# Kernel tuning notes

Hardware: AMD Instinct MI355X
Metric: run time of the kernel (lower is better)

## Reference

```python
import jax, jax.numpy as jnp
import numpy as np

N, E, IN_DIM, H, D = 50000, 1600000, 128, 4, 32
LEAKY_ALPHA = 0.2

def _glorot(key, shape):
    r = np.sqrt(6.0 / (shape[0] + shape[1]))
    return jax.random.uniform(key, shape, jnp.float32, -r, r)

def setup_inputs() -> dict:
    key = jax.random.key(0)
    ks = jax.random.split(key, 6)
    x = jax.random.normal(ks[0], (N, IN_DIM), jnp.float32)
    edge_index = jax.random.randint(ks[1], (2, E), 0, N, jnp.int64 if jax.config.jax_enable_x64 else jnp.int32)
    W_src = _glorot(ks[2], (IN_DIM, H * D))
    W_dst = _glorot(ks[3], (IN_DIM, H * D))
    W_val = _glorot(ks[4], (IN_DIM, H * D))
    attn_vec = _glorot(ks[5], (1, H)).reshape(1, H, 1) * jnp.ones((1, H, D), jnp.float32)
    # faithful glorot for (1,H,D): fan based on shape[0]+shape[1]=1+H as in source
    r = np.sqrt(6.0 / (1 + H))
    attn_vec = jax.random.uniform(jax.random.fold_in(key, 7), (1, H, D), jnp.float32, -r, r)
    return {"x": x, "edge_index": edge_index, "W_src": W_src, "W_dst": W_dst, "W_val": W_val, "attn_vec": attn_vec}

def reference(x, edge_index, W_src, W_dst, W_val, attn_vec):
    n = x.shape[0]
    h = attn_vec.shape[1]
    d = attn_vec.shape[2]
    h_s = (x @ W_src).reshape(n, h, d)
    h_d = (x @ W_dst).reshape(n, h, d)
    h_v = (x @ W_val).reshape(n, h, d)
    src, dst = edge_index[0], edge_index[1]
    # GATv2 edge scores: a^T LeakyReLU(W_src h_i + W_dst h_j)  -> [E, H]
    middle = jax.nn.leaky_relu(h_s[src] + h_d[dst], negative_slope=LEAKY_ALPHA)
    scores = jnp.sum(middle * attn_vec, axis=-1)  # [E, H]
    # segment softmax over incoming edges of each dst node (all heads at once)
    seg_max = jax.ops.segment_max(scores, dst, num_segments=n)  # [N, H]
    exp_scores = jnp.exp(scores - seg_max[dst])
    seg_sum = jax.ops.segment_sum(exp_scores, dst, num_segments=n)
    attn = exp_scores / (seg_sum[dst] + 1e-9)  # [E, H]
    # weighted message aggregation
    messages = (attn[..., None] * h_v[src]).reshape(-1, h * d)  # [E, H*D]
    out_sum = jax.ops.segment_sum(messages, dst, num_segments=n)  # [N, H*D]
    return out_sum, attn
```

## Files before the change

### kernel.cpp

```cpp
#include <hip/hip_runtime.h>

#define LEAKY 0.2f
#define BCAP 512

typedef __attribute__((ext_vector_type(8))) short short8v;
typedef __attribute__((ext_vector_type(4))) float f32x4;
typedef _Float16 half2v __attribute__((ext_vector_type(2)));

__device__ __forceinline__ float h2f(unsigned short b) {
    union { unsigned short u; _Float16 h; } c; c.u = b; return (float)c.h;
}
__device__ __forceinline__ unsigned short f2h(float f) {
    union { unsigned short u; _Float16 h; } c; c.h = (_Float16)f; return c.u;
}
__device__ __forceinline__ half2v u2h2(unsigned u) {
    union { unsigned u; half2v h; } c; c.u = u; return c.h;
}
__device__ __forceinline__ void h4w(unsigned wx, unsigned wy, float& a, float& b, float& c, float& d) {
    a = h2f((unsigned short)(wx & 0xFFFF)); b = h2f((unsigned short)(wx >> 16));
    c = h2f((unsigned short)(wy & 0xFFFF)); d = h2f((unsigned short)(wy >> 16));
}
__device__ __forceinline__ unsigned short f2bf(float f) {
    unsigned u = __float_as_uint(f);
    return (unsigned short)((u + 0x7FFFu + ((u >> 16) & 1u)) >> 16);
}
__device__ __forceinline__ float bf2f(unsigned short b) {
    return __uint_as_float((unsigned)b << 16);
}
__device__ __forceinline__ int clampi(int v, int hi) { return v < 0 ? 0 : (v > hi ? hi : v); }
__device__ __forceinline__ int ld_idx(const int* __restrict__ ei, int is64, size_t pos) {
    return is64 ? ei[pos * 2] : ei[pos];
}
__device__ __forceinline__ half2v h2max(half2v a, half2v b) {
#if __has_builtin(__builtin_elementwise_max)
    return __builtin_elementwise_max(a, b);
#else
    half2v r; r.x = a.x > b.x ? a.x : b.x; r.y = a.y > b.y ? a.y : b.y; return r;
#endif
}
__device__ __forceinline__ half2v h2min(half2v a, half2v b) {
#if __has_builtin(__builtin_elementwise_min)
    return __builtin_elementwise_min(a, b);
#else
    half2v r; r.x = a.x < b.x ? a.x : b.x; r.y = a.y < b.y ? a.y : b.y; return r;
#endif
}
__device__ __forceinline__ float fdot2f(half2v a, half2v b, float c) {
#if __has_builtin(__builtin_amdgcn_fdot2)
    return __builtin_amdgcn_fdot2(a, b, c, false);
#else
    return (float)a.x * (float)b.x + (float)a.y * (float)b.y + c;
#endif
}

__global__ __launch_bounds__(256) void prep_kernel(
    const int* __restrict__ ei, int* __restrict__ iflag,
    int* __restrict__ bcnt, int NB8,
    const float* __restrict__ W0, const float* __restrict__ W1, const float* __restrict__ W2,
    uint4* __restrict__ wfrag)
{
    const int b = blockIdx.x;
    if (b == 0) {
        __shared__ int nz;
        if (threadIdx.x == 0) nz = 0;
        __syncthreads();
        if (ei[2 * threadIdx.x + 1] != 0) atomicOr(&nz, 1);
        __syncthreads();
        if (threadIdx.x == 0) *iflag = (nz == 0) ? 1 : 0;
    } else if (b <= 24) {
        int t = (b - 1) * 256 + threadIdx.x;
        int lane = t & 63, ks = (t >> 6) & 3, nt = (t >> 8) & 7, w = t >> 11;
        const float* W = (w == 0) ? W0 : ((w == 1) ? W1 : W2);
        int col = nt * 16 + (lane & 15);
        int k0 = ks * 32 + ((lane >> 4) & 3) * 8;
        short8v h, l;
        #pragma unroll
        for (int j = 0; j < 8; ++j) {
            float v = W[(size_t)(k0 + j) * 128 + col];
            unsigned short hb = f2bf(v);
            h[j] = (short)hb;
            l[j] = (short)f2bf(v - bf2f(hb));
        }
        size_t slot = ((size_t)nt * 4 + ks) * 64 + lane;
        *(short8v*)&wfrag[(size_t)w * 4096 + 0 * 2048 + slot] = h;
        *(short8v*)&wfrag[(size_t)w * 4096 + 1 * 2048 + slot] = l;
    } else {
        int t = (b - 25) * 256 + threadIdx.x;
        if (t < NB8) bcnt[t] = 0;
    }
}

__global__ __launch_bounds__(256) void bucket_scatter_kernel(
    const int* __restrict__ ei, const int* __restrict__ iflag,
    int* __restrict__ bcnt, uint2* __restrict__ bucket_data, int N, int E)
{
    int t = blockIdx.x * 256 + threadIdx.x;
    if (t >= E) return;
    int is64 = *iflag;
    int src = clampi(ld_idx(ei, is64, (size_t)t), N - 1);
    int dst = clampi(ld_idx(ei, is64, (size_t)E + t), N - 1);
    int slot = (dst >> 6) * 8 + (blockIdx.x & 7);
    int k = atomicAdd(&bcnt[slot], 1);
    if (k < BCAP)
        bucket_data[(size_t)slot * BCAP + k] =
            make_uint2((unsigned)src | ((unsigned)(dst & 63) << 16), (unsigned)t);
}

__global__ __launch_bounds__(256) void bscan_kernel(
    const int* __restrict__ bcnt, int* __restrict__ bbase,
    int* __restrict__ offs, int NB, int N, int E)
{
    __shared__ int buf[256];
    __shared__ int base;
    const int t = threadIdx.x;
    if (t == 0) { base = 0; bbase[0] = 0; offs[N] = E; }
    __syncthreads();
    for (int start = 0; start < NB; start += 256) {
        int i = start + t;
        int v = 0;
        if (i < NB) {
            #pragma unroll
            for (int s = 0; s < 8; ++s) {
                int c = bcnt[i * 8 + s];
                v += (c < BCAP ? c : BCAP);
            }
        }
        buf[t] = v;
        __syncthreads();
        #pragma unroll
        for (int off = 1; off < 256; off <<= 1) {
            int xv = (t >= off) ? buf[t - off] : 0;
            __syncthreads();
            buf[t] += xv;
            __syncthreads();
        }
        if (i < NB) bbase[i + 1] = base + buf[t];
        __syncthreads();
        if (t == 0) base += buf[255];
        __syncthreads();
    }
}

__global__ __launch_bounds__(256) void csr_build_kernel(
    const uint2* __restrict__ bucket_data, const int* __restrict__ bcnt,
    const int* __restrict__ bbase, int* __restrict__ offs,
    int2* __restrict__ sorted2, int N)
{
    __shared__ uint2 ebuf[8 * BCAP];
    __shared__ int cnt[64];
    __shared__ int pre[64];
    __shared__ int soff[9];
    const int b = blockIdx.x;
    const int t = threadIdx.x;
    if (t == 0) {
        int acc = 0;
        #pragma unroll
        for (int s = 0; s < 8; ++s) {
            soff[s] = acc;
            int c = bcnt[b * 8 + s];
            acc += (c < BCAP ? c : BCAP);
        }
        soff[8] = acc;
    }
    if (t < 64) cnt[t] = 0;
    __syncthreads();
    const int tcnt = soff[8];
    #pragma unroll
    for (int s = 0; s < 8; ++s) {
        int o = soff[s], c = soff[s + 1] - o;
        const uint2* p = &bucket_data[((size_t)b * 8 + s) * BCAP];
        for (int k = t; k < c; k += 256) ebuf[o + k] = p[k];
    }
    __syncthreads();
    for (int k = t; k < tcnt; k += 256)
        atomicAdd(&cnt[(ebuf[k].x >> 16) & 63], 1);
    __syncthreads();
    const int gbase = bbase[b];
    if (t < 64) {
        int v = cnt[t], o = v;
        #pragma unroll
        for (int off = 1; off < 64; off <<= 1) {
            int xv = __shfl_up(v, off);
            if (t >= off) v += xv;
        }
        pre[t] = v - o;
        int node = b * 64 + t;
        if (node < N) offs[node] = gbase + pre[t];
    }
    __syncthreads();
    if (t < 64) cnt[t] = pre[t];
    __syncthreads();
    for (int k = t; k < tcnt; k += 256) {
        uint2 d = ebuf[k];
        int dl = (d.x >> 16) & 63;
        int pos = gbase + atomicAdd(&cnt[dl], 1);
        sorted2[pos] = make_int2((int)(d.x & 0xFFFF), (int)d.y);
    }
}

__global__ __launch_bounds__(256) void gemm3_mfma_kernel(
    const float* __restrict__ x, const uint4* __restrict__ wfrag,
    unsigned short* __restrict__ comb_us, float* __restrict__ hd, int N)
{
    __shared__ uint4 wsb4[4096];
    unsigned short* wsb = (unsigned short*)wsb4;
    const int tid = threadIdx.x;
    const int wave = tid >> 6;
    const int lane = tid & 63;
    const int lhi = lane >> 4;
    const int llo = lane & 15;
    const int base_row = blockIdx.x * 128 + wave * 32;

    short8v Ahi[2][4], Alo[2][4];
    #pragma unroll
    for (int rt = 0; rt < 2; ++rt) {
        #pragma unroll
        for (int ks = 0; ks < 4; ++ks) {
            int row = base_row + rt * 16 + llo;
            int rowc = row < N ? row : N - 1;
            const float* p = &x[(size_t)rowc * 128 + ks * 32 + lhi * 8];
            float4 v0 = *(const float4*)p;
            float4 v1 = *(const float4*)(p + 4);
            float vv[8] = {v0.x, v0.y, v0.z, v0.w, v1.x, v1.y, v1.z, v1.w};
            short8v h, l;
            #pragma unroll
            for (int j = 0; j < 8; ++j) {
                unsigned short hb = f2bf(vv[j]);
                h[j] = (short)hb;
                l[j] = (short)f2bf(vv[j] - bf2f(hb));
            }
            Ahi[rt][ks] = h; Alo[rt][ks] = l;
        }
    }

    for (int w = 0; w < 3; ++w) {
        __syncthreads();
        #pragma unroll
        for (int it = 0; it < 16; ++it) {
            int slot = it * 256 + tid;
            wsb4[slot] = wfrag[(size_t)w * 4096 + slot];
        }
        __syncthreads();

        f32x4 acc[2][8];
        #pragma unroll
        for (int rt = 0; rt < 2; ++rt)
            #pragma unroll
            for (int nt = 0; nt < 8; ++nt)
                acc[rt][nt] = (f32x4){0.f, 0.f, 0.f, 0.f};

        #pragma unroll
        for (int ks = 0; ks < 4; ++ks) {
            #pragma unroll
            for (int nt = 0; nt < 8; ++nt) {
                short8v Bh = *(short8v*)&wsb[((((size_t)0 * 8 + nt) * 4 + ks) * 64 + lane) * 8];
                short8v Bl = *(short8v*)&wsb[((((size_t)1 * 8 + nt) * 4 + ks) * 64 + lane) * 8];
                acc[0][nt] = __builtin_amdgcn_mfma_f32_16x16x32_bf16(Ahi[0][ks], Bh, acc[0][nt], 0, 0, 0);
                acc[1][nt] = __builtin_amdgcn_mfma_f32_16x16x32_bf16(Ahi[1][ks], Bh, acc[1][nt], 0, 0, 0);
                acc[0][nt] = __builtin_amdgcn_mfma_f32_16x16x32_bf16(Alo[0][ks], Bh, acc[0][nt], 0, 0, 0);
                acc[1][nt] = __builtin_amdgcn_mfma_f32_16x16x32_bf16(Alo[1][ks], Bh, acc[1][nt], 0, 0, 0);
                acc[0][nt] = __builtin_amdgcn_mfma_f32_16x16x32_bf16(Ahi[0][ks], Bl, acc[0][nt], 0, 0, 0);
                acc[1][nt] = __builtin_amdgcn_mfma_f32_16x16x32_bf16(Ahi[1][ks], Bl, acc[1][nt], 0, 0, 0);
            }
        }

        #pragma unroll
        for (int rt = 0; rt < 2; ++rt) {
            #pragma unroll
            for (int nt = 0; nt < 8; ++nt) {
                #pragma unroll
                for (int reg = 0; reg < 4; ++reg) {
                    int node = base_row + rt * 16 + lhi * 4 + reg;
                    int col = nt * 16 + llo;
                    if (node < N) {
                        float v = acc[rt][nt][reg];
                        if (w == 1) {
                            hd[(size_t)node * 128 + col] = v;
                        } else {
                            int slot = (w == 2) ? 1 : 0;
                            comb_us[(size_t)node * 256 + (col >> 2) * 8 + slot * 4 + (col & 3)] = f2h(v);
                        }
                    }
                }
            }
        }
    }
}

__global__ __launch_bounds__(256) void gather_fused_kernel(
    const int* __restrict__ offs, const int2* __restrict__ sorted2,
    const uint4* __restrict__ comb, const float* __restrict__ hd,
    const float* __restrict__ av,
    float* __restrict__ scores, float* __restrict__ out,
    float* __restrict__ segsum, int N)
{
    int wid = (int)(((size_t)blockIdx.x * 256 + threadIdx.x) >> 6);
    if (wid >= N) return;
    int lane = threadIdx.x & 63;
    int sub = lane >> 5;
    int le = lane & 31;
    int h = le >> 3;
    int beg = offs[wid], end = offs[wid + 1];

    float4 d4 = *(const float4*)&hd[(size_t)wid * 128 + le * 4];
    float4 a4 = *(const float4*)&av[le * 4];
    const half2v d2_0 = {(_Float16)d4.x, (_Float16)d4.y};
    const half2v d2_1 = {(_Float16)d4.z, (_Float16)d4.w};
    const half2v av2_0 = {(_Float16)a4.x, (_Float16)a4.y};
    const half2v av2_1 = {(_Float16)a4.z, (_Float16)a4.w};
    const half2v hz = {(_Float16)0.f, (_Float16)0.f};

    float sum = 0.f;
    float a0 = 0.f, a1 = 0.f, a2 = 0.f, a3 = 0.f;

    int j = beg + sub;
    int2 se0 = make_int2(0, 0), se1 = make_int2(0, 0);
    uint4 c0 = make_uint4(0, 0, 0, 0);
    if (j < end)     se0 = sorted2[j];
    if (j + 2 < end) se1 = sorted2[j + 2];
    if (j < end)     c0 = comb[(size_t)se0.x * 32 + le];

    while (j < end) {
        int jn = j + 2;
        int2 se2 = make_int2(0, 0);
        uint4 c1 = make_uint4(0, 0, 0, 0);
        if (jn + 2 < end) se2 = sorted2[jn + 2];
        if (jn < end)     c1 = comb[(size_t)se1.x * 32 + le];

        half2v m0 = u2h2(c0.x) + d2_0;
        half2v m1 = u2h2(c0.y) + d2_1;
        half2v p0 = h2max(m0, hz), q0 = h2min(m0, hz);
        half2v p1 = h2max(m1, hz), q1 = h2min(m1, hz);
        float sp = fdot2f(p1, av2_1, fdot2f(p0, av2_0, 0.f));
        float sq = fdot2f(q1, av2_1, fdot2f(q0, av2_0, 0.f));
        float s = fmaf(LEAKY, sq, sp);
        s += __shfl_xor(s, 1);
        s += __shfl_xor(s, 2);
        s += __shfl_xor(s, 4);
        float w = __expf(s);
        if ((le & 7) == 0) scores[(size_t)se0.y * 4 + h] = w;
        sum += w;
        float v0, v1, v2, v3;
        h4w(c0.z, c0.w, v0, v1, v2, v3);
        a0 += w * v0; a1 += w * v1; a2 += w * v2; a3 += w * v3;

        j = jn; se0 = se1; se1 = se2; c0 = c1;
    }
    sum += __shfl_xor(sum, 32);
    a0 += __shfl_xor(a0, 32); a1 += __shfl_xor(a1, 32);
    a2 += __shfl_xor(a2, 32); a3 += __shfl_xor(a3, 32);
    float inv = 1.f / (sum + 1e-9f);
    if (sub == 0) {
        *(float4*)&out[(size_t)wid * 128 + le * 4] =
            make_float4(a0 * inv, a1 * inv, a2 * inv, a3 * inv);
        if ((le & 7) == 0) segsum[(size_t)wid * 4 + h] = inv;
    }
}

__global__ __launch_bounds__(256) void attn_write_kernel(
    const int* __restrict__ ei, const int* __restrict__ iflag,
    float* sc, const float* __restrict__ segsum, int N, int E)
{
    int t = blockIdx.x * 256 + threadIdx.x;
    if (t >= E * 4) return;
    int e = t >> 2, h = t & 3;
    int dst = clampi(ld_idx(ei, *iflag, (size_t)E + e), N - 1);
    sc[t] = sc[t] * segsum[(size_t)dst * 4 + h];
}

extern "C" void kernel_launch(void* const* d_in, const int* in_sizes, int n_in,
                              void* d_out, int out_size, void* d_ws, size_t ws_size,
                              hipStream_t stream)
{
    const float* x  = (const float*)d_in[0];
    const int* ei   = (const int*)d_in[1];
    const float* W0 = (const float*)d_in[2];
    const float* W1 = (const float*)d_in[3];
    const float* W2 = (const float*)d_in[4];
    const float* av = (const float*)d_in[5];
    const int N = in_sizes[0] / 128;
    const int E = in_sizes[1] / 2;
    const int NB = (N + 63) >> 6;

    float* out_f = (float*)d_out;
    float* hd = out_f;
    float* out_sum = out_f;
    float* scores = out_f + (size_t)N * 128;

    uint2* bucket_data = (uint2*)d_ws;
    uint4* comb = (uint4*)d_ws;
    size_t ubytes = ((size_t)NB * 8 * BCAP * 8 + 255) & ~(size_t)255;
    int2* sorted2 = (int2*)((char*)d_ws + ubytes);
    float* segsum = (float*)(sorted2 + (size_t)E);
    int* bcnt = (int*)(segsum + (size_t)N * 4);
    int* bbase = bcnt + NB * 8;
    int* offs = bbase + (NB + 1);
    int* iflag = offs + (N + 1);
    uint4* wfrag = (uint4*)(((uintptr_t)(iflag + 1) + 255) & ~(uintptr_t)255);

    const int zblocks = (NB * 8 + 255) / 256;
    prep_kernel<<<25 + zblocks, 256, 0, stream>>>(ei, iflag, bcnt, NB * 8, W0, W1, W2, wfrag);
    bucket_scatter_kernel<<<(E + 255) / 256, 256, 0, stream>>>(
        ei, iflag, bcnt, bucket_data, N, E);
    bscan_kernel<<<1, 256, 0, stream>>>(bcnt, bbase, offs, NB, N, E);
    csr_build_kernel<<<NB, 256, 0, stream>>>(bucket_data, bcnt, bbase, offs, sorted2, N);
    gemm3_mfma_kernel<<<(N + 127) / 128, 256, 0, stream>>>(
        x, wfrag, (unsigned short*)comb, hd, N);
    gather_fused_kernel<<<(N + 3) / 4, 256, 0, stream>>>(
        offs, sorted2, comb, hd, av, scores, out_sum, segsum, N);
    attn_write_kernel<<<(E * 4 + 255) / 256, 256, 0, stream>>>(
        ei, iflag, scores, segsum, N, E);
}
```

Before: 379.5 us.

## Fuse attention normalization into gather kernel and alias bucket buffer into output

Removes the separate attn_write kernel: each node's wave now rescales its own edges' scores by the inverse segment sum right after aggregation, using the CSR edge ids instead of rereading edge_index and a segsum array. The GEMM is moved before bucketing, and the bucket staging buffer now lives in the scores region of the output, which shrinks workspace use and avoids a separate allocation. The bscan kernel uses 1024 threads and BCAP drops to 511. This relies on the waitcnt and intra-wave ordering so that each score is written before it is rescaled, and the rescale does scattered read-modify-writes on scores.

```diff
diff --git a/kernel.cpp b/kernel.cpp
--- a/kernel.cpp
+++ b/kernel.cpp
@@ -1,7 +1,7 @@
 #include <hip/hip_runtime.h>
 
 #define LEAKY 0.2f
-#define BCAP 512
+#define BCAP 511
 
 typedef __attribute__((ext_vector_type(8))) short short8v;
 typedef __attribute__((ext_vector_type(4))) float f32x4;
@@ -87,114 +87,6 @@
     } else {
         int t = (b - 25) * 256 + threadIdx.x;
         if (t < NB8) bcnt[t] = 0;
-    }
-}
-
-__global__ __launch_bounds__(256) void bucket_scatter_kernel(
-    const int* __restrict__ ei, const int* __restrict__ iflag,
-    int* __restrict__ bcnt, uint2* __restrict__ bucket_data, int N, int E)
-{
-    int t = blockIdx.x * 256 + threadIdx.x;
-    if (t >= E) return;
-    int is64 = *iflag;
-    int src = clampi(ld_idx(ei, is64, (size_t)t), N - 1);
-    int dst = clampi(ld_idx(ei, is64, (size_t)E + t), N - 1);
-    int slot = (dst >> 6) * 8 + (blockIdx.x & 7);
-    int k = atomicAdd(&bcnt[slot], 1);
-    if (k < BCAP)
-        bucket_data[(size_t)slot * BCAP + k] =
-            make_uint2((unsigned)src | ((unsigned)(dst & 63) << 16), (unsigned)t);
-}
-
-__global__ __launch_bounds__(256) void bscan_kernel(
-    const int* __restrict__ bcnt, int* __restrict__ bbase,
-    int* __restrict__ offs, int NB, int N, int E)
-{
-    __shared__ int buf[256];
-    __shared__ int base;
-    const int t = threadIdx.x;
-    if (t == 0) { base = 0; bbase[0] = 0; offs[N] = E; }
-    __syncthreads();
-    for (int start = 0; start < NB; start += 256) {
-        int i = start + t;
-        int v = 0;
-        if (i < NB) {
-            #pragma unroll
-            for (int s = 0; s < 8; ++s) {
-                int c = bcnt[i * 8 + s];
-                v += (c < BCAP ? c : BCAP);
-            }
-        }
-        buf[t] = v;
-        __syncthreads();
-        #pragma unroll
-        for (int off = 1; off < 256; off <<= 1) {
-            int xv = (t >= off) ? buf[t - off] : 0;
-            __syncthreads();
-            buf[t] += xv;
-            __syncthreads();
-        }
-        if (i < NB) bbase[i + 1] = base + buf[t];
-        __syncthreads();
-        if (t == 0) base += buf[255];
-        __syncthreads();
-    }
-}
-
-__global__ __launch_bounds__(256) void csr_build_kernel(
-    const uint2* __restrict__ bucket_data, const int* __restrict__ bcnt,
-    const int* __restrict__ bbase, int* __restrict__ offs,
-    int2* __restrict__ sorted2, int N)
-{
-    __shared__ uint2 ebuf[8 * BCAP];
-    __shared__ int cnt[64];
-    __shared__ int pre[64];
-    __shared__ int soff[9];
-    const int b = blockIdx.x;
-    const int t = threadIdx.x;
-    if (t == 0) {
-        int acc = 0;
-        #pragma unroll
-        for (int s = 0; s < 8; ++s) {
-            soff[s] = acc;
-            int c = bcnt[b * 8 + s];
-            acc += (c < BCAP ? c : BCAP);
-        }
-        soff[8] = acc;
-    }
-    if (t < 64) cnt[t] = 0;
-    __syncthreads();
-    const int tcnt = soff[8];
-    #pragma unroll
-    for (int s = 0; s < 8; ++s) {
-        int o = soff[s], c = soff[s + 1] - o;
-        const uint2* p = &bucket_data[((size_t)b * 8 + s) * BCAP];
-        for (int k = t; k < c; k += 256) ebuf[o + k] = p[k];
-    }
-    __syncthreads();
-    for (int k = t; k < tcnt; k += 256)
-        atomicAdd(&cnt[(ebuf[k].x >> 16) & 63], 1);
-    __syncthreads();
-    const int gbase = bbase[b];
-    if (t < 64) {
-        int v = cnt[t], o = v;
-        #pragma unroll
-        for (int off = 1; off < 64; off <<= 1) {
-            int xv = __shfl_up(v, off);
-            if (t >= off) v += xv;
-        }
-        pre[t] = v - o;
-        int node = b * 64 + t;
-        if (node < N) offs[node] = gbase + pre[t];
-    }
-    __syncthreads();
-    if (t < 64) cnt[t] = pre[t];
-    __syncthreads();
-    for (int k = t; k < tcnt; k += 256) {
-        uint2 d = ebuf[k];
-        int dl = (d.x >> 16) & 63;
-        int pos = gbase + atomicAdd(&cnt[dl], 1);
-        sorted2[pos] = make_int2((int)(d.x & 0xFFFF), (int)d.y);
     }
 }
 
@@ -287,12 +179,119 @@
     }
 }
 
+__global__ __launch_bounds__(256) void bucket_scatter_kernel(
+    const int* __restrict__ ei, const int* __restrict__ iflag,
+    int* __restrict__ bcnt, uint2* __restrict__ bucket_data, int N, int E)
+{
+    int t = blockIdx.x * 256 + threadIdx.x;
+    if (t >= E) return;
+    int is64 = *iflag;
+    int src = clampi(ld_idx(ei, is64, (size_t)t), N - 1);
+    int dst = clampi(ld_idx(ei, is64, (size_t)E + t), N - 1);
+    int slot = (dst >> 6) * 8 + (blockIdx.x & 7);
+    int k = atomicAdd(&bcnt[slot], 1);
+    if (k < BCAP)
+        bucket_data[(size_t)slot * BCAP + k] =
+            make_uint2((unsigned)src | ((unsigned)(dst & 63) << 16), (unsigned)t);
+}
+
+__global__ __launch_bounds__(1024) void bscan_kernel(
+    const int* __restrict__ bcnt, int* __restrict__ bbase,
+    int* __restrict__ offs, int NB, int N, int E)
+{
+    __shared__ int buf[1024];
+    __shared__ int base;
+    const int t = threadIdx.x;
+    if (t == 0) { base = 0; bbase[0] = 0; offs[N] = E; }
+    __syncthreads();
+    for (int start = 0; start < NB; start += 1024) {
+        int i = start + t;
+        int v = 0;
+        if (i < NB) {
+            #pragma unroll
+            for (int s = 0; s < 8; ++s) {
+                int c = bcnt[i * 8 + s];
+                v += (c < BCAP ? c : BCAP);
+            }
+        }
+        buf[t] = v;
+        __syncthreads();
+        #pragma unroll
+        for (int off = 1; off < 1024; off <<= 1) {
+            int xv = (t >= off) ? buf[t - off] : 0;
+            __syncthreads();
+            buf[t] += xv;
+            __syncthreads();
+        }
+        if (i < NB) bbase[i + 1] = base + buf[t];
+        __syncthreads();
+        if (t == 0) base += buf[1023];
+        __syncthreads();
+    }
+}
+
+__global__ __launch_bounds__(256) void csr_build_kernel(
+    const uint2* __restrict__ bucket_data, const int* __restrict__ bcnt,
+    const int* __restrict__ bbase, int* __restrict__ offs,
+    int2* __restrict__ sorted2, int N)
+{
+    __shared__ uint2 ebuf[8 * BCAP];
+    __shared__ int cnt[64];
+    __shared__ int pre[64];
+    __shared__ int soff[9];
+    const int b = blockIdx.x;
+    const int t = threadIdx.x;
+    if (t == 0) {
+        int acc = 0;
+        #pragma unroll
+        for (int s = 0; s < 8; ++s) {
+            soff[s] = acc;
+            int c = bcnt[b * 8 + s];
+            acc += (c < BCAP ? c : BCAP);
+        }
+        soff[8] = acc;
+    }
+    if (t < 64) cnt[t] = 0;
+    __syncthreads();
+    const int tcnt = soff[8];
+    #pragma unroll
+    for (int s = 0; s < 8; ++s) {
+        int o = soff[s], c = soff[s + 1] - o;
+        const uint2* p = &bucket_data[((size_t)b * 8 + s) * BCAP];
+        for (int k = t; k < c; k += 256) ebuf[o + k] = p[k];
+    }
+    __syncthreads();
+    for (int k = t; k < tcnt; k += 256)
+        atomicAdd(&cnt[(ebuf[k].x >> 16) & 63], 1);
+    __syncthreads();
+    const int gbase = bbase[b];
+    if (t < 64) {
+        int v = cnt[t], o = v;
+        #pragma unroll
+        for (int off = 1; off < 64; off <<= 1) {
+            int xv = __shfl_up(v, off);
+            if (t >= off) v += xv;
+        }
+        pre[t] = v - o;
+        int node = b * 64 + t;
+        if (node < N) offs[node] = gbase + pre[t];
+    }
+    __syncthreads();
+    if (t < 64) cnt[t] = pre[t];
+    __syncthreads();
+    for (int k = t; k < tcnt; k += 256) {
+        uint2 d = ebuf[k];
+        int dl = (d.x >> 16) & 63;
+        int pos = gbase + atomicAdd(&cnt[dl], 1);
+        sorted2[pos] = make_int2((int)(d.x & 0xFFFF), (int)d.y);
+    }
+}
+
 __global__ __launch_bounds__(256) void gather_fused_kernel(
     const int* __restrict__ offs, const int2* __restrict__ sorted2,
     const uint4* __restrict__ comb, const float* __restrict__ hd,
     const float* __restrict__ av,
-    float* __restrict__ scores, float* __restrict__ out,
-    float* __restrict__ segsum, int N)
+    float* __restrict__ scores, float* __restrict__ out, int N)
 {
     int wid = (int)(((size_t)blockIdx.x * 256 + threadIdx.x) >> 6);
     if (wid >= N) return;
@@ -353,19 +352,15 @@
     if (sub == 0) {
         *(float4*)&out[(size_t)wid * 128 + le * 4] =
             make_float4(a0 * inv, a1 * inv, a2 * inv, a3 * inv);
-        if ((le & 7) == 0) segsum[(size_t)wid * 4 + h] = inv;
-    }
-}
-
-__global__ __launch_bounds__(256) void attn_write_kernel(
-    const int* __restrict__ ei, const int* __restrict__ iflag,
-    float* sc, const float* __restrict__ segsum, int N, int E)
-{
-    int t = blockIdx.x * 256 + threadIdx.x;
-    if (t >= E * 4) return;
-    int e = t >> 2, h = t & 3;
-    int dst = clampi(ld_idx(ei, *iflag, (size_t)E + e), N - 1);
-    sc[t] = sc[t] * segsum[(size_t)dst * 4 + h];
+    }
+
+    asm volatile("s_waitcnt vmcnt(0)" ::: "memory");
+    float invh = __shfl(inv, (lane & 3) * 8);
+    for (int j2 = beg + (lane >> 2); j2 < end; j2 += 16) {
+        int eid = sorted2[j2].y;
+        size_t o = (size_t)eid * 4 + (lane & 3);
+        scores[o] = scores[o] * invh;
+    }
 }
 
 extern "C" void kernel_launch(void* const* d_in, const int* in_sizes, int n_in,
@@ -386,13 +381,11 @@
     float* hd = out_f;
     float* out_sum = out_f;
     float* scores = out_f + (size_t)N * 128;
-
-    uint2* bucket_data = (uint2*)d_ws;
+    uint2* bucket_data = (uint2*)scores;
+
     uint4* comb = (uint4*)d_ws;
-    size_t ubytes = ((size_t)NB * 8 * BCAP * 8 + 255) & ~(size_t)255;
-    int2* sorted2 = (int2*)((char*)d_ws + ubytes);
-    float* segsum = (float*)(sorted2 + (size_t)E);
-    int* bcnt = (int*)(segsum + (size_t)N * 4);
+    int2* sorted2 = (int2*)(comb + (size_t)N * 32);
+    int* bcnt = (int*)(sorted2 + (size_t)E);
     int* bbase = bcnt + NB * 8;
     int* offs = bbase + (NB + 1);
     int* iflag = offs + (N + 1);
@@ -400,14 +393,12 @@
 
     const int zblocks = (NB * 8 + 255) / 256;
     prep_kernel<<<25 + zblocks, 256, 0, stream>>>(ei, iflag, bcnt, NB * 8, W0, W1, W2, wfrag);
+    gemm3_mfma_kernel<<<(N + 127) / 128, 256, 0, stream>>>(
+        x, wfrag, (unsigned short*)comb, hd, N);
     bucket_scatter_kernel<<<(E + 255) / 256, 256, 0, stream>>>(
         ei, iflag, bcnt, bucket_data, N, E);
-    bscan_kernel<<<1, 256, 0, stream>>>(bcnt, bbase, offs, NB, N, E);
+    bscan_kernel<<<1, 1024, 0, stream>>>(bcnt, bbase, offs, NB, N, E);
     csr_build_kernel<<<NB, 256, 0, stream>>>(bucket_data, bcnt, bbase, offs, sorted2, N);
-    gemm3_mfma_kernel<<<(N + 127) / 128, 256, 0, stream>>>(
-        x, wfrag, (unsigned short*)comb, hd, N);
     gather_fused_kernel<<<(N + 3) / 4, 256, 0, stream>>>(
-        offs, sorted2, comb, hd, av, scores, out_sum, segsum, N);
-    attn_write_kernel<<<(E * 4 + 255) / 256, 256, 0, stream>>>(
-        ei, iflag, scores, segsum, N, E);
-}
+        offs, sorted2, comb, hd, av, scores, out_sum, N);
+}
```

Result: slower. 411.8 us (+8.5%).

## Replace CSR scan kernel with atomic cursor, store hd as fp16

Applied to the files above, without the earlier changes.

Drops the single-block prefix-scan kernel. Each CSR build block now claims its output range with an atomicAdd on a global cursor and writes (begin, end) offset pairs per node, so node segments are no longer in global order but each stays contiguous. The dst projection is stored as fp16 inside the output buffer, bucket data is moved into the scores region of the output, and the GEMM is launched before the bucket scatter. This cuts one serial launch and some memory traffic, at the cost of relying on buffer aliasing and reordered kernels being safe.

```diff
diff --git a/kernel.cpp b/kernel.cpp
--- a/kernel.cpp
+++ b/kernel.cpp
@@ -1,7 +1,7 @@
 #include <hip/hip_runtime.h>
 
 #define LEAKY 0.2f
-#define BCAP 512
+#define BCAP 511
 
 typedef __attribute__((ext_vector_type(8))) short short8v;
 typedef __attribute__((ext_vector_type(4))) float f32x4;
@@ -54,7 +54,7 @@
 }
 
 __global__ __launch_bounds__(256) void prep_kernel(
-    const int* __restrict__ ei, int* __restrict__ iflag,
+    const int* __restrict__ ei, int* __restrict__ iflag, int* __restrict__ gcursor,
     int* __restrict__ bcnt, int NB8,
     const float* __restrict__ W0, const float* __restrict__ W1, const float* __restrict__ W2,
     uint4* __restrict__ wfrag)
@@ -62,7 +62,7 @@
     const int b = blockIdx.x;
     if (b == 0) {
         __shared__ int nz;
-        if (threadIdx.x == 0) nz = 0;
+        if (threadIdx.x == 0) { nz = 0; *gcursor = 0; }
         __syncthreads();
         if (ei[2 * threadIdx.x + 1] != 0) atomicOr(&nz, 1);
         __syncthreads();
@@ -90,117 +90,9 @@
     }
 }
 
-__global__ __launch_bounds__(256) void bucket_scatter_kernel(
-    const int* __restrict__ ei, const int* __restrict__ iflag,
-    int* __restrict__ bcnt, uint2* __restrict__ bucket_data, int N, int E)
-{
-    int t = blockIdx.x * 256 + threadIdx.x;
-    if (t >= E) return;
-    int is64 = *iflag;
-    int src = clampi(ld_idx(ei, is64, (size_t)t), N - 1);
-    int dst = clampi(ld_idx(ei, is64, (size_t)E + t), N - 1);
-    int slot = (dst >> 6) * 8 + (blockIdx.x & 7);
-    int k = atomicAdd(&bcnt[slot], 1);
-    if (k < BCAP)
-        bucket_data[(size_t)slot * BCAP + k] =
-            make_uint2((unsigned)src | ((unsigned)(dst & 63) << 16), (unsigned)t);
-}
-
-__global__ __launch_bounds__(256) void bscan_kernel(
-    const int* __restrict__ bcnt, int* __restrict__ bbase,
-    int* __restrict__ offs, int NB, int N, int E)
-{
-    __shared__ int buf[256];
-    __shared__ int base;
-    const int t = threadIdx.x;
-    if (t == 0) { base = 0; bbase[0] = 0; offs[N] = E; }
-    __syncthreads();
-    for (int start = 0; start < NB; start += 256) {
-        int i = start + t;
-        int v = 0;
-        if (i < NB) {
-            #pragma unroll
-            for (int s = 0; s < 8; ++s) {
-                int c = bcnt[i * 8 + s];
-                v += (c < BCAP ? c : BCAP);
-            }
-        }
-        buf[t] = v;
-        __syncthreads();
-        #pragma unroll
-        for (int off = 1; off < 256; off <<= 1) {
-            int xv = (t >= off) ? buf[t - off] : 0;
-            __syncthreads();
-            buf[t] += xv;
-            __syncthreads();
-        }
-        if (i < NB) bbase[i + 1] = base + buf[t];
-        __syncthreads();
-        if (t == 0) base += buf[255];
-        __syncthreads();
-    }
-}
-
-__global__ __launch_bounds__(256) void csr_build_kernel(
-    const uint2* __restrict__ bucket_data, const int* __restrict__ bcnt,
-    const int* __restrict__ bbase, int* __restrict__ offs,
-    int2* __restrict__ sorted2, int N)
-{
-    __shared__ uint2 ebuf[8 * BCAP];
-    __shared__ int cnt[64];
-    __shared__ int pre[64];
-    __shared__ int soff[9];
-    const int b = blockIdx.x;
-    const int t = threadIdx.x;
-    if (t == 0) {
-        int acc = 0;
-        #pragma unroll
-        for (int s = 0; s < 8; ++s) {
-            soff[s] = acc;
-            int c = bcnt[b * 8 + s];
-            acc += (c < BCAP ? c : BCAP);
-        }
-        soff[8] = acc;
-    }
-    if (t < 64) cnt[t] = 0;
-    __syncthreads();
-    const int tcnt = soff[8];
-    #pragma unroll
-    for (int s = 0; s < 8; ++s) {
-        int o = soff[s], c = soff[s + 1] - o;
-        const uint2* p = &bucket_data[((size_t)b * 8 + s) * BCAP];
-        for (int k = t; k < c; k += 256) ebuf[o + k] = p[k];
-    }
-    __syncthreads();
-    for (int k = t; k < tcnt; k += 256)
-        atomicAdd(&cnt[(ebuf[k].x >> 16) & 63], 1);
-    __syncthreads();
-    const int gbase = bbase[b];
-    if (t < 64) {
-        int v = cnt[t], o = v;
-        #pragma unroll
-        for (int off = 1; off < 64; off <<= 1) {
-            int xv = __shfl_up(v, off);
-            if (t >= off) v += xv;
-        }
-        pre[t] = v - o;
-        int node = b * 64 + t;
-        if (node < N) offs[node] = gbase + pre[t];
-    }
-    __syncthreads();
-    if (t < 64) cnt[t] = pre[t];
-    __syncthreads();
-    for (int k = t; k < tcnt; k += 256) {
-        uint2 d = ebuf[k];
-        int dl = (d.x >> 16) & 63;
-        int pos = gbase + atomicAdd(&cnt[dl], 1);
-        sorted2[pos] = make_int2((int)(d.x & 0xFFFF), (int)d.y);
-    }
-}
-
 __global__ __launch_bounds__(256) void gemm3_mfma_kernel(
     const float* __restrict__ x, const uint4* __restrict__ wfrag,
-    unsigned short* __restrict__ comb_us, float* __restrict__ hd, int N)
+    unsigned short* __restrict__ comb_us, unsigned short* __restrict__ hdh, int N)
 {
     __shared__ uint4 wsb4[4096];
     unsigned short* wsb = (unsigned short*)wsb4;
@@ -275,7 +167,7 @@
                     if (node < N) {
                         float v = acc[rt][nt][reg];
                         if (w == 1) {
-                            hd[(size_t)node * 128 + col] = v;
+                            hdh[(size_t)node * 256 + col] = f2h(v);
                         } else {
                             int slot = (w == 2) ? 1 : 0;
                             comb_us[(size_t)node * 256 + (col >> 2) * 8 + slot * 4 + (col & 3)] = f2h(v);
@@ -287,9 +179,84 @@
     }
 }
 
+__global__ __launch_bounds__(256) void bucket_scatter_kernel(
+    const int* __restrict__ ei, const int* __restrict__ iflag,
+    int* __restrict__ bcnt, uint2* __restrict__ bucket_data, int N, int E)
+{
+    int t = blockIdx.x * 256 + threadIdx.x;
+    if (t >= E) return;
+    int is64 = *iflag;
+    int src = clampi(ld_idx(ei, is64, (size_t)t), N - 1);
+    int dst = clampi(ld_idx(ei, is64, (size_t)E + t), N - 1);
+    int slot = (dst >> 6) * 8 + (blockIdx.x & 7);
+    int k = atomicAdd(&bcnt[slot], 1);
+    if (k < BCAP)
+        bucket_data[(size_t)slot * BCAP + k] =
+            make_uint2((unsigned)src | ((unsigned)(dst & 63) << 16), (unsigned)t);
+}
+
+__global__ __launch_bounds__(256) void csr_build_kernel(
+    const uint2* __restrict__ bucket_data, const int* __restrict__ bcnt,
+    int* __restrict__ gcursor, int2* __restrict__ offs2,
+    int2* __restrict__ sorted2, int N)
+{
+    __shared__ uint2 ebuf[8 * BCAP];
+    __shared__ int cnt[64];
+    __shared__ int pre[64];
+    __shared__ int soff[9];
+    __shared__ int gbase_s;
+    const int b = blockIdx.x;
+    const int t = threadIdx.x;
+    if (t == 0) {
+        int acc = 0;
+        #pragma unroll
+        for (int s = 0; s < 8; ++s) {
+            soff[s] = acc;
+            int c = bcnt[b * 8 + s];
+            acc += (c < BCAP ? c : BCAP);
+        }
+        soff[8] = acc;
+        gbase_s = atomicAdd(gcursor, acc);
+    }
+    if (t < 64) cnt[t] = 0;
+    __syncthreads();
+    const int tcnt = soff[8];
+    const int gbase = gbase_s;
+    #pragma unroll
+    for (int s = 0; s < 8; ++s) {
+        int o = soff[s], c = soff[s + 1] - o;
+        const uint2* p = &bucket_data[((size_t)b * 8 + s) * BCAP];
+        for (int k = t; k < c; k += 256) ebuf[o + k] = p[k];
+    }
+    __syncthreads();
+    for (int k = t; k < tcnt; k += 256)
+        atomicAdd(&cnt[(ebuf[k].x >> 16) & 63], 1);
+    __syncthreads();
+    if (t < 64) {
+        int v = cnt[t], o = v;
+        #pragma unroll
+        for (int off = 1; off < 64; off <<= 1) {
+            int xv = __shfl_up(v, off);
+            if (t >= off) v += xv;
+        }
+        pre[t] = v - o;
+        int node = b * 64 + t;
+        if (node < N) offs2[node] = make_int2(gbase + v - o, gbase + v);
+    }
+    __syncthreads();
+    if (t < 64) cnt[t] = pre[t];
+    __syncthreads();
+    for (int k = t; k < tcnt; k += 256) {
+        uint2 d = ebuf[k];
+        int dl = (d.x >> 16) & 63;
+        int pos = gbase + atomicAdd(&cnt[dl], 1);
+        sorted2[pos] = make_int2((int)(d.x & 0xFFFF), (int)d.y);
+    }
+}
+
 __global__ __launch_bounds__(256) void gather_fused_kernel(
-    const int* __restrict__ offs, const int2* __restrict__ sorted2,
-    const uint4* __restrict__ comb, const float* __restrict__ hd,
+    const int2* __restrict__ offs2, const int2* __restrict__ sorted2,
+    const uint4* __restrict__ comb, const unsigned short* __restrict__ hdh,
     const float* __restrict__ av,
     float* __restrict__ scores, float* __restrict__ out,
     float* __restrict__ segsum, int N)
@@ -300,12 +267,13 @@
     int sub = lane >> 5;
     int le = lane & 31;
     int h = le >> 3;
-    int beg = offs[wid], end = offs[wid + 1];
-
-    float4 d4 = *(const float4*)&hd[(size_t)wid * 128 + le * 4];
+    int2 be = offs2[wid];
+    int beg = be.x, end = be.y;
+
+    uint2 hw = *(const uint2*)&hdh[(size_t)wid * 256 + le * 4];
     float4 a4 = *(const float4*)&av[le * 4];
-    const half2v d2_0 = {(_Float16)d4.x, (_Float16)d4.y};
-    const half2v d2_1 = {(_Float16)d4.z, (_Float16)d4.w};
+    const half2v d2_0 = u2h2(hw.x);
+    const half2v d2_1 = u2h2(hw.y);
     const half2v av2_0 = {(_Float16)a4.x, (_Float16)a4.y};
     const half2v av2_1 = {(_Float16)a4.z, (_Float16)a4.w};
     const half2v hz = {(_Float16)0.f, (_Float16)0.f};
@@ -383,31 +351,31 @@
     const int NB = (N + 63) >> 6;
 
     float* out_f = (float*)d_out;
-    float* hd = out_f;
+    unsigned short* hdh = (unsigned short*)out_f;
     float* out_sum = out_f;
     float* scores = out_f + (size_t)N * 128;
-
-    uint2* bucket_data = (uint2*)d_ws;
+    uint2* bucket_data = (uint2*)scores;
+
     uint4* comb = (uint4*)d_ws;
-    size_t ubytes = ((size_t)NB * 8 * BCAP * 8 + 255) & ~(size_t)255;
-    int2* sorted2 = (int2*)((char*)d_ws + ubytes);
+    int2* sorted2 = (int2*)(comb + (size_t)N * 32);
     float* segsum = (float*)(sorted2 + (size_t)E);
-    int* bcnt = (int*)(segsum + (size_t)N * 4);
-    int* bbase = bcnt + NB * 8;
-    int* offs = bbase + (NB + 1);
-    int* iflag = offs + (N + 1);
-    uint4* wfrag = (uint4*)(((uintptr_t)(iflag + 1) + 255) & ~(uintptr_t)255);
+    int2* offs2 = (int2*)(segsum + (size_t)N * 4);
+    int* bcnt = (int*)(offs2 + N);
+    int* iflag = bcnt + NB * 8;
+    int* gcursor = iflag + 1;
+    uint4* wfrag = (uint4*)(((uintptr_t)(gcursor + 1) + 255) & ~(uintptr_t)255);
 
     const int zblocks = (NB * 8 + 255) / 256;
-    prep_kernel<<<25 + zblocks, 256, 0, stream>>>(ei, iflag, bcnt, NB * 8, W0, W1, W2, wfrag);
+    prep_kernel<<<25 + zblocks, 256, 0, stream>>>(
+        ei, iflag, gcursor, bcnt, NB * 8, W0, W1, W2, wfrag);
+    gemm3_mfma_kernel<<<(N + 127) / 128, 256, 0, stream>>>(
+        x, wfrag, (unsigned short*)comb, hdh, N);
     bucket_scatter_kernel<<<(E + 255) / 256, 256, 0, stream>>>(
         ei, iflag, bcnt, bucket_data, N, E);
-    bscan_kernel<<<1, 256, 0, stream>>>(bcnt, bbase, offs, NB, N, E);
-    csr_build_kernel<<<NB, 256, 0, stream>>>(bucket_data, bcnt, bbase, offs, sorted2, N);
-    gemm3_mfma_kernel<<<(N + 127) / 128, 256, 0, stream>>>(
-        x, wfrag, (unsigned short*)comb, hd, N);
+    csr_build_kernel<<<NB, 256, 0, stream>>>(
+        bucket_data, bcnt, gcursor, offs2, sorted2, N);
     gather_fused_kernel<<<(N + 3) / 4, 256, 0, stream>>>(
-        offs, sorted2, comb, hd, av, scores, out_sum, segsum, N);
+        offs2, sorted2, comb, hdh, av, scores, out_sum, segsum, N);
     attn_write_kernel<<<(E * 4 + 255) / 256, 256, 0, stream>>>(
         ei, iflag, scores, segsum, N, E);
 }
```

Result: no change. 377.7 us (-0.5%).
